# Kernel optimization log

Measured on AMD Instinct MI355X. Metric: run time of the kernel, lower is better.

Reference implementation:

```python
import jax, jax.numpy as jnp
import numpy as np

B, D, H = 1024, 128, 128
LN_EPS = 1e-5


def setup_inputs() -> dict:
    key = jax.random.key(0)
    ks = jax.random.split(key, 12)
    s_d = 1.0 / np.sqrt(D)
    s_h = 1.0 / np.sqrt(H)
    return {
        "x": jax.random.normal(ks[0], (B, D), dtype=jnp.float32),
        # diff_proj: Linear(D, H)
        "Wd": jax.random.uniform(ks[1], (H, D), jnp.float32, -s_d, s_d),
        "bd": jax.random.uniform(ks[2], (H,), jnp.float32, -s_d, s_d),
        # tau_proj: Linear(D, 1) -> Softplus
        "Wt": jax.random.uniform(ks[3], (1, D), jnp.float32, -s_d, s_d),
        "bt": jax.random.uniform(ks[4], (1,), jnp.float32, -s_d, s_d),
        # agg: Linear(H, H) -> ReLU
        "Wa": jax.random.uniform(ks[5], (H, H), jnp.float32, -s_h, s_h),
        "ba": jax.random.uniform(ks[6], (H,), jnp.float32, -s_h, s_h),
        # res_proj: Linear(D, H)
        "Wr": jax.random.uniform(ks[7], (H, D), jnp.float32, -s_d, s_d),
        "br": jax.random.uniform(ks[8], (H,), jnp.float32, -s_d, s_d),
        # LayerNorm(H)
        "gamma": jnp.ones((H,), jnp.float32),
        "beta": jnp.zeros((H,), jnp.float32),
    }


def reference(x, Wd, bd, Wt, bt, Wa, ba, Wr, br, gamma, beta):
    # mean_j diff_proj(|x_i - x_j|) == diff_proj(mean_j |x_i - x_j|) since Linear is affine
    diffs_mean = jnp.mean(jnp.abs(x[:, None, :] - x[None, :, :]), axis=1)  # [B, D]
    d_mean = diffs_mean @ Wd.T + bd                                         # [B, H]
    # tau = softplus(x Wt^T + bt).clamp(min=0.01) + 1.0
    tau = jnp.clip(jax.nn.softplus(x @ Wt.T + bt), 0.01, None) + 1.0        # [B, 1]
    h_mean = d_mean / tau
    h = jax.nn.relu(h_mean @ Wa.T + ba)
    y = h + x @ Wr.T + br
    mu = jnp.mean(y, axis=-1, keepdims=True)
    var = jnp.var(y, axis=-1, keepdims=True)
    return (y - mu) / jnp.sqrt(var + LN_EPS) * gamma + beta
```

## Files before the change

### kernel.cpp

```cpp
#include <hip/hip_runtime.h>
#include <math.h>

#define Bn 1024
#define Dn 128
#define Hn 128

__global__ __launch_bounds__(1024) void fused_resd1(
    const float* __restrict__ x,
    const float* __restrict__ Wd, const float* __restrict__ bd,
    const float* __restrict__ Wt, const float* __restrict__ bt,
    const float* __restrict__ Wa, const float* __restrict__ ba,
    const float* __restrict__ Wr, const float* __restrict__ br,
    const float* __restrict__ gamma, const float* __restrict__ beta,
    float* __restrict__ out) {
  const int t = threadIdx.x;
  const int c = t & 31;
  const int g = t >> 5;
  const int i0 = blockIdx.x << 2;

  __shared__ float red[32][4][Dn];
  __shared__ float xs[4][Dn];
  __shared__ float dms[4][Dn];
  __shared__ float ms[4][Hn];
  __shared__ float ys[4][Hn];
  __shared__ float wt_s[Dn];
  __shared__ float tau_s[4];

  float4 xi[4];
#pragma unroll
  for (int r = 0; r < 4; ++r)
    xi[r] = *(const float4*)(x + (size_t)(i0 + r) * Dn + c * 4);

  float4 acc[4];
#pragma unroll
  for (int r = 0; r < 4; ++r) acc[r] = make_float4(0.f, 0.f, 0.f, 0.f);

  const float4* xq = (const float4*)x + (size_t)g * 32 * (Dn / 4) + c;
#pragma unroll 1
  for (int jj = 0; jj < 32; jj += 8) {
    float4 xj[8];
#pragma unroll
    for (int u = 0; u < 8; ++u) xj[u] = xq[(size_t)(jj + u) * (Dn / 4)];
#pragma unroll
    for (int u = 0; u < 8; ++u) {
#pragma unroll
      for (int r = 0; r < 4; ++r) {
        acc[r].x += fabsf(xi[r].x - xj[u].x);
        acc[r].y += fabsf(xi[r].y - xj[u].y);
        acc[r].z += fabsf(xi[r].z - xj[u].z);
        acc[r].w += fabsf(xi[r].w - xj[u].w);
      }
    }
  }
#pragma unroll
  for (int r = 0; r < 4; ++r) *(float4*)&red[g][r][c * 4] = acc[r];
  __syncthreads();

  if (t < 512) {
    const int r = t >> 7, d = t & 127;
    float s = 0.f;
#pragma unroll
    for (int gg = 0; gg < 32; ++gg) s += red[gg][r][d];
    dms[r][d] = s * (1.0f / 1024.0f);
    xs[r][d] = x[(size_t)(i0 + r) * Dn + d];
  } else if (t < 640) {
    wt_s[t - 512] = Wt[t - 512];
  }
  __syncthreads();

  if (t < 256) {
    const int r = t >> 6, p = t & 63;
    float partial = xs[r][p] * wt_s[p] + xs[r][p + 64] * wt_s[p + 64];
#pragma unroll
    for (int off = 32; off; off >>= 1) partial += __shfl_xor(partial, off, 64);
    if (p == 0) {
      const float z = partial + bt[0];
      const float sp = fmaxf(z, 0.f) + log1pf(expf(-fabsf(z)));
      tau_s[r] = 1.0f / (fmaxf(sp, 0.01f) + 1.0f);
    }
  }
  __syncthreads();

  if (t < 256) {
    const int h = t & 127;
    const int g4 = t >> 7;
    const int r0 = 2 * g4, r1 = 2 * g4 + 1;
    float m0 = bd[h], m1 = m0;
    const float4* w = (const float4*)(Wd + (size_t)h * Dn);
#pragma unroll 4
    for (int k4 = 0; k4 < Dn / 4; ++k4) {
      const float4 wv = w[k4];
      const int k = k4 * 4;
      m0 += wv.x * dms[r0][k] + wv.y * dms[r0][k + 1] + wv.z * dms[r0][k + 2] + wv.w * dms[r0][k + 3];
      m1 += wv.x * dms[r1][k] + wv.y * dms[r1][k + 1] + wv.z * dms[r1][k + 2] + wv.w * dms[r1][k + 3];
    }
    ms[r0][h] = m0 * tau_s[r0];
    ms[r1][h] = m1 * tau_s[r1];
  }
  __syncthreads();

  if (t < 256) {
    const int h = t & 127;
    const int g4 = t >> 7;
    const int r0 = 2 * g4, r1 = 2 * g4 + 1;
    float q0 = ba[h], q1 = q0, c0 = br[h], c1 = c0;
    const float4* wa = (const float4*)(Wa + (size_t)h * Dn);
    const float4* wr = (const float4*)(Wr + (size_t)h * Dn);
#pragma unroll 4
    for (int k4 = 0; k4 < Dn / 4; ++k4) {
      const float4 av = wa[k4];
      const float4 rv = wr[k4];
      const int k = k4 * 4;
      q0 += av.x * ms[r0][k] + av.y * ms[r0][k + 1] + av.z * ms[r0][k + 2] + av.w * ms[r0][k + 3];
      q1 += av.x * ms[r1][k] + av.y * ms[r1][k + 1] + av.z * ms[r1][k + 2] + av.w * ms[r1][k + 3];
      c0 += rv.x * xs[r0][k] + rv.y * xs[r0][k + 1] + rv.z * xs[r0][k + 2] + rv.w * xs[r0][k + 3];
      c1 += rv.x * xs[r1][k] + rv.y * xs[r1][k + 1] + rv.z * xs[r1][k + 2] + rv.w * xs[r1][k + 3];
    }
    ys[r0][h] = fmaxf(q0, 0.f) + c0;
    ys[r1][h] = fmaxf(q1, 0.f) + c1;
  }
  __syncthreads();

  if (t < 256) {
    const int r = t >> 6, p = t & 63;
    const float v0 = ys[r][p], v1 = ys[r][p + 64];
    float s = v0 + v1;
    float q = v0 * v0 + v1 * v1;
#pragma unroll
    for (int off = 32; off; off >>= 1) {
      s += __shfl_xor(s, off, 64);
      q += __shfl_xor(q, off, 64);
    }
    const float mu = s * (1.0f / 128.0f);
    const float var = q * (1.0f / 128.0f) - mu * mu;
    const float rs = rsqrtf(var + 1e-5f);
    float* o = out + (size_t)(i0 + r) * Hn;
    o[p]      = (v0 - mu) * rs * gamma[p]      + beta[p];
    o[p + 64] = (v1 - mu) * rs * gamma[p + 64] + beta[p + 64];
  }
}

extern "C" void kernel_launch(void* const* d_in, const int* in_sizes, int n_in,
                              void* d_out, int out_size, void* d_ws, size_t ws_size,
                              hipStream_t stream) {
  const float* x     = (const float*)d_in[0];
  const float* Wd    = (const float*)d_in[1];
  const float* bd    = (const float*)d_in[2];
  const float* Wt    = (const float*)d_in[3];
  const float* bt    = (const float*)d_in[4];
  const float* Wa    = (const float*)d_in[5];
  const float* ba    = (const float*)d_in[6];
  const float* Wr    = (const float*)d_in[7];
  const float* br    = (const float*)d_in[8];
  const float* gamma = (const float*)d_in[9];
  const float* beta  = (const float*)d_in[10];
  float* out = (float*)d_out;

  fused_resd1<<<Bn / 4, 1024, 0, stream>>>(x, Wd, bd, Wt, bt, Wa, ba, Wr, br,
                                           gamma, beta, out);
  (void)in_sizes; (void)n_in; (void)out_size; (void)d_ws; (void)ws_size;
}
```

Before: 95.51 us.

## Compute mean absolute pairwise differences via per-column bitonic sort and prefix sums

Replaces the O(B^2·D) brute-force pairwise |x_i - x_j| accumulation with a per-column bitonic sort of 1024 values and a prefix-sum formula, giving O(B log^2 B) work per column. Each of 128 blocks sorts one column using a wave shuffle for small strides and shared memory for large ones, then writes the per-row mean into a workspace buffer. A second, slimmer 256-thread kernel reads that buffer and performs the linear, softplus, ReLU and LayerNorm tail. This costs an extra launch, a workspace round trip, and many barriers in the sort, and the float prefix sums may change rounding slightly.

Measured after the change: 100.2 us. +4.9%, slower.

```diff
diff --git a/kernel.cpp b/kernel.cpp
--- a/kernel.cpp
+++ b/kernel.cpp
@@ -5,8 +5,72 @@
 #define Dn 128
 #define Hn 128
 
-__global__ __launch_bounds__(1024) void fused_resd1(
-    const float* __restrict__ x,
+__global__ __launch_bounds__(1024) void col_sort_dmean(
+    const float* __restrict__ x, float* __restrict__ dmean) {
+  const int d = blockIdx.x;
+  const int t = threadIdx.x;
+
+  __shared__ unsigned long long kvs[Bn];
+  __shared__ float wsum[16];
+
+  const float v0 = x[(size_t)t * Dn + d];
+  const unsigned int u = __float_as_uint(v0);
+  const unsigned int key = u ^ ((u >> 31) ? 0xFFFFFFFFu : 0x80000000u);
+  unsigned long long kv = ((unsigned long long)key << 32) | (unsigned int)t;
+
+#pragma unroll
+  for (int k = 2; k <= Bn; k <<= 1) {
+#pragma unroll
+    for (int j = k >> 1; j > 0; j >>= 1) {
+      unsigned long long other;
+      if (j >= 64) {
+        kvs[t] = kv;
+        __syncthreads();
+        other = kvs[t ^ j];
+        __syncthreads();
+      } else {
+        other = __shfl_xor(kv, j, 64);
+      }
+      const bool up = ((t & k) == 0);
+      const bool lowHalf = ((t & j) == 0);
+      const bool keepMin = (up == lowHalf);
+      const bool otherSmaller = (other < kv);
+      if (keepMin == otherSmaller) kv = other;
+    }
+  }
+
+  const unsigned int skey = (unsigned int)(kv >> 32);
+  const unsigned int orig = (unsigned int)(kv & 0xFFFFFFFFu);
+  const unsigned int ub =
+      (skey & 0x80000000u) ? (skey ^ 0x80000000u) : ~skey;
+  const float sv = __uint_as_float(ub);
+
+  const int lane = t & 63;
+  const int wv = t >> 6;
+  float ps = sv;
+#pragma unroll
+  for (int off = 1; off < 64; off <<= 1) {
+    const float n = __shfl_up(ps, off, 64);
+    if (lane >= off) ps += n;
+  }
+  if (lane == 63) wsum[wv] = ps;
+  __syncthreads();
+  float woff = 0.f, tot = 0.f;
+#pragma unroll
+  for (int w = 0; w < 16; ++w) {
+    const float s = wsum[w];
+    tot += s;
+    if (w < wv) woff += s;
+  }
+  const float pexcl = (ps - sv) + woff;
+
+  const float res =
+      ((float)(2 * t - Bn) * sv + tot - 2.0f * pexcl) * (1.0f / (float)Bn);
+  dmean[(size_t)orig * Dn + d] = res;
+}
+
+__global__ __launch_bounds__(256) void fused_tail(
+    const float* __restrict__ x, const float* __restrict__ dmean,
     const float* __restrict__ Wd, const float* __restrict__ bd,
     const float* __restrict__ Wt, const float* __restrict__ bt,
     const float* __restrict__ Wa, const float* __restrict__ ba,
@@ -14,11 +78,8 @@
     const float* __restrict__ gamma, const float* __restrict__ beta,
     float* __restrict__ out) {
   const int t = threadIdx.x;
-  const int c = t & 31;
-  const int g = t >> 5;
   const int i0 = blockIdx.x << 2;
 
-  __shared__ float red[32][4][Dn];
   __shared__ float xs[4][Dn];
   __shared__ float dms[4][Dn];
   __shared__ float ms[4][Hn];
@@ -26,49 +87,16 @@
   __shared__ float wt_s[Dn];
   __shared__ float tau_s[4];
 
-  float4 xi[4];
-#pragma unroll
-  for (int r = 0; r < 4; ++r)
-    xi[r] = *(const float4*)(x + (size_t)(i0 + r) * Dn + c * 4);
-
-  float4 acc[4];
-#pragma unroll
-  for (int r = 0; r < 4; ++r) acc[r] = make_float4(0.f, 0.f, 0.f, 0.f);
-
-  const float4* xq = (const float4*)x + (size_t)g * 32 * (Dn / 4) + c;
-#pragma unroll 1
-  for (int jj = 0; jj < 32; jj += 8) {
-    float4 xj[8];
-#pragma unroll
-    for (int u = 0; u < 8; ++u) xj[u] = xq[(size_t)(jj + u) * (Dn / 4)];
-#pragma unroll
-    for (int u = 0; u < 8; ++u) {
-#pragma unroll
-      for (int r = 0; r < 4; ++r) {
-        acc[r].x += fabsf(xi[r].x - xj[u].x);
-        acc[r].y += fabsf(xi[r].y - xj[u].y);
-        acc[r].z += fabsf(xi[r].z - xj[u].z);
-        acc[r].w += fabsf(xi[r].w - xj[u].w);
-      }
-    }
-  }
-#pragma unroll
-  for (int r = 0; r < 4; ++r) *(float4*)&red[g][r][c * 4] = acc[r];
-  __syncthreads();
-
-  if (t < 512) {
-    const int r = t >> 7, d = t & 127;
-    float s = 0.f;
-#pragma unroll
-    for (int gg = 0; gg < 32; ++gg) s += red[gg][r][d];
-    dms[r][d] = s * (1.0f / 1024.0f);
-    xs[r][d] = x[(size_t)(i0 + r) * Dn + d];
-  } else if (t < 640) {
-    wt_s[t - 512] = Wt[t - 512];
+  {
+    const int r = t >> 6, p2 = (t & 63) << 1;
+    *(float2*)&xs[r][p2] = *(const float2*)(x + (size_t)(i0 + r) * Dn + p2);
+    *(float2*)&dms[r][p2] =
+        *(const float2*)(dmean + (size_t)(i0 + r) * Dn + p2);
+    if (t < Dn) wt_s[t] = Wt[t];
   }
   __syncthreads();
 
-  if (t < 256) {
+  {
     const int r = t >> 6, p = t & 63;
     float partial = xs[r][p] * wt_s[p] + xs[r][p + 64] * wt_s[p + 64];
 #pragma unroll
@@ -81,7 +109,7 @@
   }
   __syncthreads();
 
-  if (t < 256) {
+  {
     const int h = t & 127;
     const int g4 = t >> 7;
     const int r0 = 2 * g4, r1 = 2 * g4 + 1;
@@ -91,15 +119,17 @@
     for (int k4 = 0; k4 < Dn / 4; ++k4) {
       const float4 wv = w[k4];
       const int k = k4 * 4;
-      m0 += wv.x * dms[r0][k] + wv.y * dms[r0][k + 1] + wv.z * dms[r0][k + 2] + wv.w * dms[r0][k + 3];
-      m1 += wv.x * dms[r1][k] + wv.y * dms[r1][k + 1] + wv.z * dms[r1][k + 2] + wv.w * dms[r1][k + 3];
+      m0 += wv.x * dms[r0][k] + wv.y * dms[r0][k + 1] + wv.z * dms[r0][k + 2] +
+            wv.w * dms[r0][k + 3];
+      m1 += wv.x * dms[r1][k] + wv.y * dms[r1][k + 1] + wv.z * dms[r1][k + 2] +
+            wv.w * dms[r1][k + 3];
     }
     ms[r0][h] = m0 * tau_s[r0];
     ms[r1][h] = m1 * tau_s[r1];
   }
   __syncthreads();
 
-  if (t < 256) {
+  {
     const int h = t & 127;
     const int g4 = t >> 7;
     const int r0 = 2 * g4, r1 = 2 * g4 + 1;
@@ -111,17 +141,21 @@
       const float4 av = wa[k4];
       const float4 rv = wr[k4];
       const int k = k4 * 4;
-      q0 += av.x * ms[r0][k] + av.y * ms[r0][k + 1] + av.z * ms[r0][k + 2] + av.w * ms[r0][k + 3];
-      q1 += av.x * ms[r1][k] + av.y * ms[r1][k + 1] + av.z * ms[r1][k + 2] + av.w * ms[r1][k + 3];
-      c0 += rv.x * xs[r0][k] + rv.y * xs[r0][k + 1] + rv.z * xs[r0][k + 2] + rv.w * xs[r0][k + 3];
-      c1 += rv.x * xs[r1][k] + rv.y * xs[r1][k + 1] + rv.z * xs[r1][k + 2] + rv.w * xs[r1][k + 3];
+      q0 += av.x * ms[r0][k] + av.y * ms[r0][k + 1] + av.z * ms[r0][k + 2] +
+            av.w * ms[r0][k + 3];
+      q1 += av.x * ms[r1][k] + av.y * ms[r1][k + 1] + av.z * ms[r1][k + 2] +
+            av.w * ms[r1][k + 3];
+      c0 += rv.x * xs[r0][k] + rv.y * xs[r0][k + 1] + rv.z * xs[r0][k + 2] +
+            rv.w * xs[r0][k + 3];
+      c1 += rv.x * xs[r1][k] + rv.y * xs[r1][k + 1] + rv.z * xs[r1][k + 2] +
+            rv.w * xs[r1][k + 3];
     }
     ys[r0][h] = fmaxf(q0, 0.f) + c0;
     ys[r1][h] = fmaxf(q1, 0.f) + c1;
   }
   __syncthreads();
 
-  if (t < 256) {
+  {
     const int r = t >> 6, p = t & 63;
     const float v0 = ys[r][p], v1 = ys[r][p + 64];
     float s = v0 + v1;
@@ -135,28 +169,30 @@
     const float var = q * (1.0f / 128.0f) - mu * mu;
     const float rs = rsqrtf(var + 1e-5f);
     float* o = out + (size_t)(i0 + r) * Hn;
-    o[p]      = (v0 - mu) * rs * gamma[p]      + beta[p];
+    o[p] = (v0 - mu) * rs * gamma[p] + beta[p];
     o[p + 64] = (v1 - mu) * rs * gamma[p + 64] + beta[p + 64];
   }
 }
 
 extern "C" void kernel_launch(void* const* d_in, const int* in_sizes, int n_in,
-                              void* d_out, int out_size, void* d_ws, size_t ws_size,
-                              hipStream_t stream) {
-  const float* x     = (const float*)d_in[0];
-  const float* Wd    = (const float*)d_in[1];
-  const float* bd    = (const float*)d_in[2];
-  const float* Wt    = (const float*)d_in[3];
-  const float* bt    = (const float*)d_in[4];
-  const float* Wa    = (const float*)d_in[5];
-  const float* ba    = (const float*)d_in[6];
-  const float* Wr    = (const float*)d_in[7];
-  const float* br    = (const float*)d_in[8];
+                              void* d_out, int out_size, void* d_ws,
+                              size_t ws_size, hipStream_t stream) {
+  const float* x = (const float*)d_in[0];
+  const float* Wd = (const float*)d_in[1];
+  const float* bd = (const float*)d_in[2];
+  const float* Wt = (const float*)d_in[3];
+  const float* bt = (const float*)d_in[4];
+  const float* Wa = (const float*)d_in[5];
+  const float* ba = (const float*)d_in[6];
+  const float* Wr = (const float*)d_in[7];
+  const float* br = (const float*)d_in[8];
   const float* gamma = (const float*)d_in[9];
-  const float* beta  = (const float*)d_in[10];
+  const float* beta = (const float*)d_in[10];
   float* out = (float*)d_out;
+  float* dmean = (float*)d_ws;
 
-  fused_resd1<<<Bn / 4, 1024, 0, stream>>>(x, Wd, bd, Wt, bt, Wa, ba, Wr, br,
-                                           gamma, beta, out);
-  (void)in_sizes; (void)n_in; (void)out_size; (void)d_ws; (void)ws_size;
+  col_sort_dmean<<<Dn, Bn, 0, stream>>>(x, dmean);
+  fused_tail<<<Bn / 4, 256, 0, stream>>>(x, dmean, Wd, bd, Wt, bt, Wa, ba, Wr,
+                                         br, gamma, beta, out);
+  (void)in_sizes; (void)n_in; (void)out_size; (void)ws_size;
 }
```

## Spread epilogue GEMVs across all threads and merge reduction via shuffles

Applied to the files above, without the earlier changes.

The pairwise-distance partial sums from the two 32-lane halves of each wavefront are now combined with a cross-lane shuffle, which halves the shared reduction buffer and the later reduction loop. The x-row and Wt staging moves before the main loop, and the tau computation runs alongside the dms reduction, removing one barrier. The Wd and Wa GEMVs now use 512 threads with one row each instead of 256 threads with two rows. The residual Wr GEMV is moved onto the other 512 threads so it runs concurrently with the Wd stage. This increases parallelism in the epilogue, at the cost of each weight row being loaded by more threads.

Result: slower. 107.5 us (+12.5%).

```diff
diff --git a/kernel.cpp b/kernel.cpp
--- a/kernel.cpp
+++ b/kernel.cpp
@@ -18,11 +18,12 @@
   const int g = t >> 5;
   const int i0 = blockIdx.x << 2;
 
-  __shared__ float red[32][4][Dn];
+  __shared__ float red[16][4][Dn];
   __shared__ float xs[4][Dn];
   __shared__ float dms[4][Dn];
   __shared__ float ms[4][Hn];
-  __shared__ float ys[4][Hn];
+  __shared__ float ysq[4][Hn];
+  __shared__ float ysc[4][Hn];
   __shared__ float wt_s[Dn];
   __shared__ float tau_s[4];
 
@@ -30,6 +31,9 @@
 #pragma unroll
   for (int r = 0; r < 4; ++r)
     xi[r] = *(const float4*)(x + (size_t)(i0 + r) * Dn + c * 4);
+
+  if (g < 4) *(float4*)&xs[g][c * 4] = xi[g];
+  if (t >= 128 && t < 256) wt_s[t - 128] = Wt[t - 128];
 
   float4 acc[4];
 #pragma unroll
@@ -52,24 +56,30 @@
       }
     }
   }
+
 #pragma unroll
-  for (int r = 0; r < 4; ++r) *(float4*)&red[g][r][c * 4] = acc[r];
+  for (int r = 0; r < 4; ++r) {
+    acc[r].x += __shfl_xor(acc[r].x, 32, 64);
+    acc[r].y += __shfl_xor(acc[r].y, 32, 64);
+    acc[r].z += __shfl_xor(acc[r].z, 32, 64);
+    acc[r].w += __shfl_xor(acc[r].w, 32, 64);
+  }
+  if ((t & 32) == 0) {
+    const int w = g >> 1;
+#pragma unroll
+    for (int r = 0; r < 4; ++r) *(float4*)&red[w][r][c * 4] = acc[r];
+  }
   __syncthreads();
 
   if (t < 512) {
     const int r = t >> 7, d = t & 127;
     float s = 0.f;
 #pragma unroll
-    for (int gg = 0; gg < 32; ++gg) s += red[gg][r][d];
+    for (int gg = 0; gg < 16; ++gg) s += red[gg][r][d];
     dms[r][d] = s * (1.0f / 1024.0f);
-    xs[r][d] = x[(size_t)(i0 + r) * Dn + d];
-  } else if (t < 640) {
-    wt_s[t - 512] = Wt[t - 512];
-  }
-  __syncthreads();
-
-  if (t < 256) {
-    const int r = t >> 6, p = t & 63;
+  } else if (t < 768) {
+    const int tt = t - 512;
+    const int r = tt >> 6, p = tt & 63;
     float partial = xs[r][p] * wt_s[p] + xs[r][p + 64] * wt_s[p + 64];
 #pragma unroll
     for (int off = 32; off; off >>= 1) partial += __shfl_xor(partial, off, 64);
@@ -81,49 +91,53 @@
   }
   __syncthreads();
 
-  if (t < 256) {
-    const int h = t & 127;
-    const int g4 = t >> 7;
-    const int r0 = 2 * g4, r1 = 2 * g4 + 1;
-    float m0 = bd[h], m1 = m0;
+  if (t < 512) {
+    const int r = t >> 7, h = t & 127;
+    float m = bd[h];
     const float4* w = (const float4*)(Wd + (size_t)h * Dn);
 #pragma unroll 4
     for (int k4 = 0; k4 < Dn / 4; ++k4) {
       const float4 wv = w[k4];
       const int k = k4 * 4;
-      m0 += wv.x * dms[r0][k] + wv.y * dms[r0][k + 1] + wv.z * dms[r0][k + 2] + wv.w * dms[r0][k + 3];
-      m1 += wv.x * dms[r1][k] + wv.y * dms[r1][k + 1] + wv.z * dms[r1][k + 2] + wv.w * dms[r1][k + 3];
+      m += wv.x * dms[r][k] + wv.y * dms[r][k + 1] + wv.z * dms[r][k + 2] +
+           wv.w * dms[r][k + 3];
     }
-    ms[r0][h] = m0 * tau_s[r0];
-    ms[r1][h] = m1 * tau_s[r1];
+    ms[r][h] = m * tau_s[r];
+  } else {
+    const int tt = t - 512;
+    const int r = tt >> 7, h = tt & 127;
+    float cc = br[h];
+    const float4* w = (const float4*)(Wr + (size_t)h * Dn);
+#pragma unroll 4
+    for (int k4 = 0; k4 < Dn / 4; ++k4) {
+      const float4 wv = w[k4];
+      const int k = k4 * 4;
+      cc += wv.x * xs[r][k] + wv.y * xs[r][k + 1] + wv.z * xs[r][k + 2] +
+            wv.w * xs[r][k + 3];
+    }
+    ysc[r][h] = cc;
   }
   __syncthreads();
 
-  if (t < 256) {
-    const int h = t & 127;
-    const int g4 = t >> 7;
-    const int r0 = 2 * g4, r1 = 2 * g4 + 1;
-    float q0 = ba[h], q1 = q0, c0 = br[h], c1 = c0;
-    const float4* wa = (const float4*)(Wa + (size_t)h * Dn);
-    const float4* wr = (const float4*)(Wr + (size_t)h * Dn);
+  if (t < 512) {
+    const int r = t >> 7, h = t & 127;
+    float q = ba[h];
+    const float4* w = (const float4*)(Wa + (size_t)h * Dn);
 #pragma unroll 4
     for (int k4 = 0; k4 < Dn / 4; ++k4) {
-      const float4 av = wa[k4];
-      const float4 rv = wr[k4];
+      const float4 wv = w[k4];
       const int k = k4 * 4;
-      q0 += av.x * ms[r0][k] + av.y * ms[r0][k + 1] + av.z * ms[r0][k + 2] + av.w * ms[r0][k + 3];
-      q1 += av.x * ms[r1][k] + av.y * ms[r1][k + 1] + av.z * ms[r1][k + 2] + av.w * ms[r1][k + 3];
-      c0 += rv.x * xs[r0][k] + rv.y * xs[r0][k + 1] + rv.z * xs[r0][k + 2] + rv.w * xs[r0][k + 3];
-      c1 += rv.x * xs[r1][k] + rv.y * xs[r1][k + 1] + rv.z * xs[r1][k + 2] + rv.w * xs[r1][k + 3];
+      q += wv.x * ms[r][k] + wv.y * ms[r][k + 1] + wv.z * ms[r][k + 2] +
+           wv.w * ms[r][k + 3];
     }
-    ys[r0][h] = fmaxf(q0, 0.f) + c0;
-    ys[r1][h] = fmaxf(q1, 0.f) + c1;
+    ysq[r][h] = fmaxf(q, 0.f);
   }
   __syncthreads();
 
   if (t < 256) {
     const int r = t >> 6, p = t & 63;
-    const float v0 = ys[r][p], v1 = ys[r][p + 64];
+    const float v0 = ysq[r][p] + ysc[r][p];
+    const float v1 = ysq[r][p + 64] + ysc[r][p + 64];
     float s = v0 + v1;
     float q = v0 * v0 + v1 * v1;
 #pragma unroll
@@ -141,8 +155,8 @@
 }
 
 extern "C" void kernel_launch(void* const* d_in, const int* in_sizes, int n_in,
-                              void* d_out, int out_size, void* d_ws, size_t ws_size,
-                              hipStream_t stream) {
+                              void* d_out, int out_size, void* d_ws,
+                              size_t ws_size, hipStream_t stream) {
   const float* x     = (const float*)d_in[0];
   const float* Wd    = (const float*)d_in[1];
   const float* bd    = (const float*)d_in[2];
```
